# Performance work log

Measured on AMD Instinct MI355X. Metric: run time of the kernel, lower is better.

## Reference

```python
import jax, jax.numpy as jnp
import numpy as np

N, F, C, H, D = 32768, 128, 4, 8, 32
DM = H * D  # 256, d_model
E, B = 65536, 8192


def _pe():
    # sinusoidal positional encoding over the chain dimension, shape [C, DM]
    pos = jnp.arange(C, dtype=jnp.float32)[:, None]
    di = jnp.arange(0, DM, 2, dtype=jnp.float32)[None, :]
    div = 10000.0 ** (di / DM)
    pe = jnp.zeros((C, DM), jnp.float32)
    pe = pe.at[:, 0::2].set(jnp.sin(pos / div))
    pe = pe.at[:, 1::2].set(jnp.cos(pos / div))
    return pe


def _leaky(v):
    return jnp.where(v >= 0, v, 0.2 * v)


def setup_inputs() -> dict:
    key = jax.random.key(0)
    ks = jax.random.split(key, 6)
    x = jax.random.normal(ks[0], (N, F), jnp.float32)
    edge_index = jax.random.randint(ks[1], (2, E), 0, N)
    bridge_index = jax.random.randint(ks[2], (2, B), 0, N)
    W_in = jax.random.normal(ks[3], (DM, F), jnp.float32) * 0.05       # linear_input.weight
    double_attn = jax.random.normal(ks[4], (1, C * H, D), jnp.float32) * 0.1
    W_res = jax.random.normal(ks[5], (C * DM, F), jnp.float32) * 0.05  # residual_linear.weight
    bias = jnp.zeros((C * DM,), jnp.float32)
    prelu_w = jnp.float32(0.25)  # nn.PReLU default
    return {"x": x, "edge_index": edge_index, "bridge_index": bridge_index,
            "W_in": W_in, "double_attn": double_attn, "W_res": W_res,
            "bias": bias, "prelu_w": prelu_w}


def reference(x, edge_index, bridge_index, W_in, double_attn, W_res, bias, prelu_w):
    n = x.shape[0]
    # project + chain positional encoding -> [n, C, H, D]
    xl = x @ W_in.T                                   # [n, DM]
    xr = (xl[:, None, :] + _pe()[None]).reshape(n, C, H, D)

    src_bond, dst_bond = edge_index[0], edge_index[1]
    bond_attn = _leaky(xr[src_bond] + xr[dst_bond])   # [E, C, H, D]

    src_bridge, dst_bridge = bridge_index[0], bridge_index[1]
    ch = jnp.arange(C)
    prev_ch = jnp.clip(ch - 1, 0, None)
    next_ch = jnp.clip(ch + 1, None, C - 1)
    src2dst = _leaky(xr[dst_bridge] + xr[src_bridge][:, next_ch]).at[:, -1].set(0.0)
    dst2src = _leaky(xr[src_bridge] + xr[dst_bridge][:, prev_ch]).at[:, 0].set(0.0)

    full_src = jnp.concatenate([src_bond, src_bridge, dst_bridge])   # [Et]
    full_dst = jnp.concatenate([dst_bond, dst_bridge, src_bridge])   # [Et]
    x_src = jnp.concatenate([xr[src_bond], xr[src_bridge], xr[dst_bridge]], axis=0).reshape(-1, C * H, D)
    edge_attn = jnp.concatenate([bond_attn, src2dst, dst2src], axis=0).reshape(-1, C * H, D)

    scores = (double_attn * edge_attn).sum(-1)        # [Et, C*H]
    exp_s = jnp.exp(scores - scores.max())            # global-max stabilized, as in original
    denom = jax.ops.segment_sum(exp_s, full_dst, num_segments=n)     # [n, C*H]
    alpha = exp_s / (denom[full_dst] + 1e-16)

    # NOTE: faithful to original bug - x_src (per-edge, len Et) indexed by NODE ids
    proj = x_src[full_src] * alpha[..., None]         # [Et, C*H, D]
    out = jax.ops.segment_sum(proj, full_dst, num_segments=n)        # [n, C*H, D]

    out = out + (x @ W_res.T).reshape(n, C * H, D)    # residual
    out = out.reshape(n, C * H * D) + bias            # concat + bias
    out = jnp.where(out >= 0, out, prelu_w * out)     # PReLU
    return out
```

## Files before the change

### kernel.cpp

```cpp
#include <hip/hip_runtime.h>
#include <math.h>

#define N_NODES 32768
#define F_IN    128
#define C_CH    4
#define H_HEADS 8
#define D_DIM   32
#define DM      256
#define E_BOND  65536
#define B_BRIDGE 8192
#define ET      (E_BOND + 2*B_BRIDGE)
#define OUTC    1024
#define CAP     24
#define NCOLS   1280

#define WS_XL      0u
#define WS_PE      33554432u
#define WS_BUCKET4 33558528u
#define WS_CNT     46141440u
#define WS_RESID   46272512u
#define WS_XB      113381376u
#define WS_WC      121769984u

typedef __attribute__((ext_vector_type(8))) short bf16x8;
typedef __attribute__((ext_vector_type(4))) float f32x4;
typedef __attribute__((ext_vector_type(4))) _Float16 f16x4;

__device__ __forceinline__ float leaky(float v) { return v >= 0.f ? v : 0.2f*v; }
__device__ __forceinline__ ushort f2bf(float f) {
    unsigned u = __float_as_uint(f);
    unsigned r = (u + 0x7fffu + ((u >> 16) & 1u)) >> 16;
    return (ushort)r;
}

__device__ __forceinline__ void edge_decode(int e, const int* __restrict__ ei,
                                            const int* __restrict__ bi,
                                            int& nA, int& nB, int& tp) {
    if (e < E_BOND)               { nA = ei[e]; nB = ei[E_BOND + e]; tp = 0; }
    else if (e < E_BOND+B_BRIDGE) { int i = e - E_BOND;
                                    nA = bi[B_BRIDGE + i]; nB = bi[i]; tp = 1; }
    else                          { int i = e - E_BOND - B_BRIDGE;
                                    nA = bi[i]; nB = bi[B_BRIDGE + i]; tp = 2; }
}

__global__ __launch_bounds__(256) void prep_kernel(
        const float* __restrict__ x, const float* __restrict__ W_in,
        const float* __restrict__ W_res, const int* __restrict__ ei,
        const int* __restrict__ bi, ushort* __restrict__ xb,
        ushort* __restrict__ wc, int* __restrict__ counts,
        int4* __restrict__ bucket4, float* __restrict__ pe) {
    const int bid = blockIdx.x;
    const int tid = threadIdx.x;
    if (bid < 4096) {
        const long i = (long)bid*256 + tid;
        float4 v = ((const float4*)x)[i];
        ushort4 o; o.x = f2bf(v.x); o.y = f2bf(v.y); o.z = f2bf(v.z); o.w = f2bf(v.w);
        ((ushort4*)xb)[i] = o;
    } else if (bid < 4256) {
        const int i = (bid - 4096)*256 + tid;
        float4 v = (i < 8192) ? ((const float4*)W_in)[i]
                              : ((const float4*)W_res)[i - 8192];
        ushort4 o; o.x = f2bf(v.x); o.y = f2bf(v.y); o.z = f2bf(v.z); o.w = f2bf(v.w);
        ((ushort4*)wc)[i] = o;
    } else if (bid < 4576) {
        const int e = (bid - 4256)*256 + tid;
        if (e < ET) {
            int nA, nB, tp;
            edge_decode(e, ei, bi, nA, nB, tp);
            const int dst = (tp == 0) ? nB : nA;
            const int fs  = (tp == 0) ? nA : nB;
            const int g   = ei[fs];
            int slot = atomicAdd(&counts[dst], 1);
            if (slot < CAP) bucket4[(long)dst*CAP + slot] = make_int4(nA, nB, g, tp);
        }
    } else {
#pragma unroll
        for (int k = 0; k < 4; ++k) {
            int idx = k*256 + tid;
            int c = idx >> 8, p = idx & 255;
            float expo = (float)(p & ~1) * (1.0f/256.0f);
            float div  = powf(10000.0f, expo);
            float arg  = (float)c / div;
            pe[idx] = (p & 1) ? cosf(arg) : sinf(arg);
        }
    }
}

#define LDSK 72
__global__ __launch_bounds__(256) void mfma_gemm(
        const ushort* __restrict__ xb, const ushort* __restrict__ wc,
        float* __restrict__ xl, _Float16* __restrict__ resid) {
    __shared__ ushort As[128*LDSK];
    __shared__ ushort Bs[128*LDSK];
    const int tid = threadIdx.x;
    const int m0 = blockIdx.x * 128;
    const int n0 = blockIdx.y * 128;
    const int lane = tid & 63, wv = tid >> 6;
    const int wm = wv & 1, wn = wv >> 1;
    const int quad = lane >> 4, l15 = lane & 15;
    const int mbase = wm*64, nbase = wn*64;
    f32x4 acc[4][4] = {};

    for (int kt = 0; kt < 2; ++kt) {
        if (kt) __syncthreads();
#pragma unroll
        for (int i = 0; i < 4; ++i) {
            int c = tid + i*256;
            int row = c >> 3, seg = c & 7;
            *(uint4*)&As[row*LDSK + seg*8] =
                *(const uint4*)(xb + (long)(m0 + row)*F_IN + kt*64 + seg*8);
        }
#pragma unroll
        for (int i = 0; i < 4; ++i) {
            int c = tid + i*256;
            int row = c >> 3, seg = c & 7;
            *(uint4*)&Bs[row*LDSK + seg*8] =
                *(const uint4*)(wc + (long)(n0 + row)*F_IN + kt*64 + seg*8);
        }
        __syncthreads();
#pragma unroll
        for (int ks = 0; ks < 2; ++ks) {
            const int ko = ks*32 + quad*8;
            bf16x8 af[4], bfr[4];
#pragma unroll
            for (int mi = 0; mi < 4; ++mi)
                af[mi] = *(const bf16x8*)&As[(mbase + mi*16 + l15)*LDSK + ko];
#pragma unroll
            for (int ni = 0; ni < 4; ++ni)
                bfr[ni] = *(const bf16x8*)&Bs[(nbase + ni*16 + l15)*LDSK + ko];
#pragma unroll
            for (int mi = 0; mi < 4; ++mi)
#pragma unroll
                for (int ni = 0; ni < 4; ++ni)
                    acc[mi][ni] = __builtin_amdgcn_mfma_f32_16x16x32_bf16(
                        af[mi], bfr[ni], acc[mi][ni], 0, 0, 0);
        }
    }

    if (n0 < DM) {
#pragma unroll
        for (int mi = 0; mi < 4; ++mi) {
            const int mrow = m0 + mbase + mi*16 + quad*4;
#pragma unroll
            for (int ni = 0; ni < 4; ++ni) {
                const int col = n0 + nbase + ni*16 + l15;
#pragma unroll
                for (int r = 0; r < 4; ++r)
                    xl[(long)(mrow + r)*DM + col] = acc[mi][ni][r];
            }
        }
    } else {
        const int coloff = n0 - DM;
#pragma unroll
        for (int mi = 0; mi < 4; ++mi) {
            const int mrow = m0 + mbase + mi*16 + quad*4;
#pragma unroll
            for (int ni = 0; ni < 4; ++ni) {
                const int col = coloff + nbase + ni*16 + l15;
#pragma unroll
                for (int r = 0; r < 4; ++r)
                    resid[(long)(mrow + r)*OUTC + col] = (_Float16)acc[mi][ni][r];
            }
        }
    }
}

__global__ __launch_bounds__(256) void node_kernel(
        const float* __restrict__ xl, const float* __restrict__ pe,
        const float* __restrict__ datt, const int* __restrict__ counts,
        const int4* __restrict__ bucket4, const _Float16* __restrict__ resid,
        const float* __restrict__ bias, const float* __restrict__ pw,
        float* __restrict__ out) {
    const int t = threadIdx.x;
    const int l = t & 63, wv = t >> 6;
    const int n = blockIdx.x*4 + wv;
    const int pos = l * 4;
    const int h = l >> 3, dq = l & 7;
    const int cnt = min(counts[n], CAP);
    const long nb = (long)n*CAP;

    float4 pv[4], w4[4];
#pragma unroll
    for (int c = 0; c < 4; ++c) {
        pv[c] = *(const float4*)(pe + c*DM + pos);
        w4[c] = *(const float4*)(datt + (c*H_HEADS + h)*D_DIM + dq*4);
    }
    f16x4 hv[4]; float4 bv[4];
#pragma unroll
    for (int c = 0; c < 4; ++c) {
        hv[c] = *(const f16x4*)(resid + (long)n*OUTC + c*256 + pos);
        bv[c] = *(const float4*)(bias + c*256 + pos);
    }
    const float w = *pw;

    float m[4]   = {-1e30f, -1e30f, -1e30f, -1e30f};
    float den[4] = {0.f, 0.f, 0.f, 0.f};
    f32x4 acc[4] = {};

    int4 ed;
    if (cnt > 0) ed = bucket4[nb];
    for (int i = 0; i < cnt; ++i) {
        const float4 ua = *(const float4*)(xl + (long)ed.x*DM + pos);
        const float4 ub = *(const float4*)(xl + (long)ed.y*DM + pos);
        const float4 xv = *(const float4*)(xl + (long)ed.z*DM + pos);
        const int tp = ed.w;
        const int nx = (i+1 < cnt) ? i+1 : i;
        ed = bucket4[nb + nx];

        const float sx = ua.x + ub.x;
        const float sy = ua.y + ub.y;
        const float sz = ua.z + ub.z;
        const float sw = ua.w + ub.w;

        float p[4];
#pragma unroll
        for (int c = 0; c < 4; ++c) {
            int cB = (tp == 0) ? c : (tp == 1 ? (c+1 < 3 ? c+1 : 3)
                                              : (c-1 > 0 ? c-1 : 0));
            bool z = (tp == 1 && c == 3) || (tp == 2 && c == 0);
            float4 pa = pv[c];
            float4 pb = (cB == 0) ? pv[0] : (cB == 1) ? pv[1]
                       : (cB == 2) ? pv[2] : pv[3];
            float v0 = leaky(sx + pa.x + pb.x);
            float v1 = leaky(sy + pa.y + pb.y);
            float v2 = leaky(sz + pa.z + pb.z);
            float v3 = leaky(sw + pa.w + pb.w);
            float d = w4[c].x*v0 + w4[c].y*v1 + w4[c].z*v2 + w4[c].w*v3;
            p[c] = z ? 0.f : d;
            p[c] += __shfl_xor(p[c], 1);
            p[c] += __shfl_xor(p[c], 2);
            p[c] += __shfl_xor(p[c], 4);
        }
#pragma unroll
        for (int c = 0; c < 4; ++c) {
            float mn   = fmaxf(m[c], p[c]);
            float corr = __expf(m[c] - mn);
            float ww   = __expf(p[c] - mn);
            den[c] = den[c]*corr + ww;
            acc[c].x = acc[c].x*corr + ww*xv.x;
            acc[c].y = acc[c].y*corr + ww*xv.y;
            acc[c].z = acc[c].z*corr + ww*xv.z;
            acc[c].w = acc[c].w*corr + ww*xv.w;
            m[c] = mn;
        }
    }

#pragma unroll
    for (int c = 0; c < 4; ++c) {
        const float inv = 1.f / (den[c] + 1e-16f);
        float r0 = (acc[c].x + den[c]*pv[c].x)*inv + (float)hv[c].x + bv[c].x;
        float r1 = (acc[c].y + den[c]*pv[c].y)*inv + (float)hv[c].y + bv[c].y;
        float r2 = (acc[c].z + den[c]*pv[c].z)*inv + (float)hv[c].z + bv[c].z;
        float r3 = (acc[c].w + den[c]*pv[c].w)*inv + (float)hv[c].w + bv[c].w;
        r0 = r0 >= 0.f ? r0 : w*r0;
        r1 = r1 >= 0.f ? r1 : w*r1;
        r2 = r2 >= 0.f ? r2 : w*r2;
        r3 = r3 >= 0.f ? r3 : w*r3;
        *(float4*)(out + (long)n*OUTC + c*256 + pos) = make_float4(r0, r1, r2, r3);
    }
}

extern "C" void kernel_launch(void* const* d_in, const int* in_sizes, int n_in,
                              void* d_out, int out_size, void* d_ws, size_t ws_size,
                              hipStream_t stream) {
    const float* x     = (const float*)d_in[0];
    const int*   ei    = (const int*)d_in[1];
    const int*   bi    = (const int*)d_in[2];
    const float* W_in  = (const float*)d_in[3];
    const float* datt  = (const float*)d_in[4];
    const float* W_res = (const float*)d_in[5];
    const float* bias  = (const float*)d_in[6];
    const float* pw    = (const float*)d_in[7];
    float* out = (float*)d_out;
    char*  ws  = (char*)d_ws;

    float*     xl      = (float*)(ws + WS_XL);
    float*     pe      = (float*)(ws + WS_PE);
    int4*      bucket4 = (int4*)(ws + WS_BUCKET4);
    int*       counts  = (int*)(ws + WS_CNT);
    _Float16*  resid   = (_Float16*)(ws + WS_RESID);
    ushort*    xb      = (ushort*)(ws + WS_XB);
    ushort*    wc      = (ushort*)(ws + WS_WC);

    hipMemsetAsync(counts, 0, (size_t)N_NODES*4, stream);
    prep_kernel<<<4577, 256, 0, stream>>>(x, W_in, W_res, ei, bi, xb, wc,
                                          counts, bucket4, pe);
    {
        dim3 grid(N_NODES/128, NCOLS/128);
        mfma_gemm<<<grid, 256, 0, stream>>>(xb, wc, xl, resid);
    }
    node_kernel<<<N_NODES/4, 256, 0, stream>>>(xl, pe, datt, counts, bucket4,
                                               resid, bias, pw, out);
}
```

Measured before the change: 332.6 us.

## Gather bf16 score features, unroll edges by two, persistent node waves

The GEMM now also writes a bf16 copy of the projected features. The node kernel gathers the two score operands from that copy, which halves their bytes, while still reading the aggregated value in fp32. The edge loop is unrolled by two to put more independent gathers in flight, and the node kernel becomes a grid-stride loop over 2048 blocks so per-wave constants load once. This adds an extra 16MB write in the GEMM and bf16 rounding in the attention scores.

```diff
diff --git a/kernel.cpp b/kernel.cpp
--- a/kernel.cpp
+++ b/kernel.cpp
@@ -15,12 +15,13 @@
 #define NCOLS   1280
 
 #define WS_XL      0u
-#define WS_PE      33554432u
-#define WS_BUCKET4 33558528u
-#define WS_CNT     46141440u
-#define WS_RESID   46272512u
-#define WS_XB      113381376u
-#define WS_WC      121769984u
+#define WS_XLB     33554432u
+#define WS_PE      50331648u
+#define WS_BUCKET4 50335744u
+#define WS_CNT     62918656u
+#define WS_RESID   63049728u
+#define WS_XB      130158592u
+#define WS_WC      138547200u
 
 typedef __attribute__((ext_vector_type(8))) short bf16x8;
 typedef __attribute__((ext_vector_type(4))) float f32x4;
@@ -31,6 +32,9 @@
     unsigned u = __float_as_uint(f);
     unsigned r = (u + 0x7fffu + ((u >> 16) & 1u)) >> 16;
     return (ushort)r;
+}
+__device__ __forceinline__ float bf2f(ushort u) {
+    return __uint_as_float((unsigned)u << 16);
 }
 
 __device__ __forceinline__ void edge_decode(int e, const int* __restrict__ ei,
@@ -89,7 +93,8 @@
 #define LDSK 72
 __global__ __launch_bounds__(256) void mfma_gemm(
         const ushort* __restrict__ xb, const ushort* __restrict__ wc,
-        float* __restrict__ xl, _Float16* __restrict__ resid) {
+        float* __restrict__ xl, ushort* __restrict__ xlb,
+        _Float16* __restrict__ resid) {
     __shared__ ushort As[128*LDSK];
     __shared__ ushort Bs[128*LDSK];
     const int tid = threadIdx.x;
@@ -145,8 +150,11 @@
             for (int ni = 0; ni < 4; ++ni) {
                 const int col = n0 + nbase + ni*16 + l15;
 #pragma unroll
-                for (int r = 0; r < 4; ++r)
-                    xl[(long)(mrow + r)*DM + col] = acc[mi][ni][r];
+                for (int r = 0; r < 4; ++r) {
+                    float v = acc[mi][ni][r];
+                    xl [(long)(mrow + r)*DM + col] = v;
+                    xlb[(long)(mrow + r)*DM + col] = f2bf(v);
+                }
             }
         }
     } else {
@@ -166,97 +174,149 @@
 }
 
 __global__ __launch_bounds__(256) void node_kernel(
-        const float* __restrict__ xl, const float* __restrict__ pe,
-        const float* __restrict__ datt, const int* __restrict__ counts,
-        const int4* __restrict__ bucket4, const _Float16* __restrict__ resid,
-        const float* __restrict__ bias, const float* __restrict__ pw,
-        float* __restrict__ out) {
+        const float* __restrict__ xl, const ushort* __restrict__ xlb,
+        const float* __restrict__ pe, const float* __restrict__ datt,
+        const int* __restrict__ counts, const int4* __restrict__ bucket4,
+        const _Float16* __restrict__ resid, const float* __restrict__ bias,
+        const float* __restrict__ pw, float* __restrict__ out) {
     const int t = threadIdx.x;
     const int l = t & 63, wv = t >> 6;
-    const int n = blockIdx.x*4 + wv;
+    const int nwaves = gridDim.x * 4;
+    const int wgid = blockIdx.x*4 + wv;
     const int pos = l * 4;
     const int h = l >> 3, dq = l & 7;
-    const int cnt = min(counts[n], CAP);
-    const long nb = (long)n*CAP;
-
-    float4 pv[4], w4[4];
+
+    float4 pv[4], w4[4], bv[4];
 #pragma unroll
     for (int c = 0; c < 4; ++c) {
         pv[c] = *(const float4*)(pe + c*DM + pos);
         w4[c] = *(const float4*)(datt + (c*H_HEADS + h)*D_DIM + dq*4);
-    }
-    f16x4 hv[4]; float4 bv[4];
-#pragma unroll
-    for (int c = 0; c < 4; ++c) {
-        hv[c] = *(const f16x4*)(resid + (long)n*OUTC + c*256 + pos);
         bv[c] = *(const float4*)(bias + c*256 + pos);
     }
     const float w = *pw;
 
-    float m[4]   = {-1e30f, -1e30f, -1e30f, -1e30f};
-    float den[4] = {0.f, 0.f, 0.f, 0.f};
-    f32x4 acc[4] = {};
-
-    int4 ed;
-    if (cnt > 0) ed = bucket4[nb];
-    for (int i = 0; i < cnt; ++i) {
-        const float4 ua = *(const float4*)(xl + (long)ed.x*DM + pos);
-        const float4 ub = *(const float4*)(xl + (long)ed.y*DM + pos);
-        const float4 xv = *(const float4*)(xl + (long)ed.z*DM + pos);
-        const int tp = ed.w;
-        const int nx = (i+1 < cnt) ? i+1 : i;
-        ed = bucket4[nb + nx];
-
-        const float sx = ua.x + ub.x;
-        const float sy = ua.y + ub.y;
-        const float sz = ua.z + ub.z;
-        const float sw = ua.w + ub.w;
-
-        float p[4];
+    for (int n = wgid; n < N_NODES; n += nwaves) {
+        const int cnt = min(counts[n], CAP);
+        const long nb = (long)n*CAP;
+
+        f16x4 hv[4];
+#pragma unroll
+        for (int c = 0; c < 4; ++c)
+            hv[c] = *(const f16x4*)(resid + (long)n*OUTC + c*256 + pos);
+
+        float m[4]   = {-1e30f, -1e30f, -1e30f, -1e30f};
+        float den[4] = {0.f, 0.f, 0.f, 0.f};
+        f32x4 acc[4] = {};
+
+        int4 edA, edB;
+        if (cnt > 0) edA = bucket4[nb];
+        if (cnt > 1) edB = bucket4[nb + 1];
+
+        for (int i = 0; i < cnt; i += 2) {
+            const ushort4 uaA = *(const ushort4*)(xlb + (long)edA.x*DM + pos);
+            const ushort4 ubA = *(const ushort4*)(xlb + (long)edA.y*DM + pos);
+            const float4  xvA = *(const float4*)(xl + (long)edA.z*DM + pos);
+            const int tpA = edA.w;
+            const bool hasB = (i + 1) < cnt;
+            ushort4 uaB, ubB; float4 xvB; int tpB = 0;
+            if (hasB) {
+                uaB = *(const ushort4*)(xlb + (long)edB.x*DM + pos);
+                ubB = *(const ushort4*)(xlb + (long)edB.y*DM + pos);
+                xvB = *(const float4*)(xl + (long)edB.z*DM + pos);
+                tpB = edB.w;
+            }
+            if (i + 2 < cnt) edA = bucket4[nb + i + 2];
+            if (i + 3 < cnt) edB = bucket4[nb + i + 3];
+
+            {
+                const float sx = bf2f(uaA.x) + bf2f(ubA.x);
+                const float sy = bf2f(uaA.y) + bf2f(ubA.y);
+                const float sz = bf2f(uaA.z) + bf2f(ubA.z);
+                const float sw = bf2f(uaA.w) + bf2f(ubA.w);
+                float p[4];
+#pragma unroll
+                for (int c = 0; c < 4; ++c) {
+                    int cB = (tpA == 0) ? c : (tpA == 1 ? (c+1 < 3 ? c+1 : 3)
+                                                        : (c-1 > 0 ? c-1 : 0));
+                    bool z = (tpA == 1 && c == 3) || (tpA == 2 && c == 0);
+                    float4 pa = pv[c];
+                    float4 pb = (cB == 0) ? pv[0] : (cB == 1) ? pv[1]
+                               : (cB == 2) ? pv[2] : pv[3];
+                    float v0 = leaky(sx + pa.x + pb.x);
+                    float v1 = leaky(sy + pa.y + pb.y);
+                    float v2 = leaky(sz + pa.z + pb.z);
+                    float v3 = leaky(sw + pa.w + pb.w);
+                    float d = w4[c].x*v0 + w4[c].y*v1 + w4[c].z*v2 + w4[c].w*v3;
+                    p[c] = z ? 0.f : d;
+                    p[c] += __shfl_xor(p[c], 1);
+                    p[c] += __shfl_xor(p[c], 2);
+                    p[c] += __shfl_xor(p[c], 4);
+                }
+#pragma unroll
+                for (int c = 0; c < 4; ++c) {
+                    float mn   = fmaxf(m[c], p[c]);
+                    float corr = __expf(m[c] - mn);
+                    float ww   = __expf(p[c] - mn);
+                    den[c] = den[c]*corr + ww;
+                    acc[c].x = acc[c].x*corr + ww*xvA.x;
+                    acc[c].y = acc[c].y*corr + ww*xvA.y;
+                    acc[c].z = acc[c].z*corr + ww*xvA.z;
+                    acc[c].w = acc[c].w*corr + ww*xvA.w;
+                    m[c] = mn;
+                }
+            }
+            if (hasB) {
+                const float sx = bf2f(uaB.x) + bf2f(ubB.x);
+                const float sy = bf2f(uaB.y) + bf2f(ubB.y);
+                const float sz = bf2f(uaB.z) + bf2f(ubB.z);
+                const float sw = bf2f(uaB.w) + bf2f(ubB.w);
+                float p[4];
+#pragma unroll
+                for (int c = 0; c < 4; ++c) {
+                    int cB = (tpB == 0) ? c : (tpB == 1 ? (c+1 < 3 ? c+1 : 3)
+                                                        : (c-1 > 0 ? c-1 : 0));
+                    bool z = (tpB == 1 && c == 3) || (tpB == 2 && c == 0);
+                    float4 pa = pv[c];
+                    float4 pb = (cB == 0) ? pv[0] : (cB == 1) ? pv[1]
+                               : (cB == 2) ? pv[2] : pv[3];
+                    float v0 = leaky(sx + pa.x + pb.x);
+                    float v1 = leaky(sy + pa.y + pb.y);
+                    float v2 = leaky(sz + pa.z + pb.z);
+                    float v3 = leaky(sw + pa.w + pb.w);
+                    float d = w4[c].x*v0 + w4[c].y*v1 + w4[c].z*v2 + w4[c].w*v3;
+                    p[c] = z ? 0.f : d;
+                    p[c] += __shfl_xor(p[c], 1);
+                    p[c] += __shfl_xor(p[c], 2);
+                    p[c] += __shfl_xor(p[c], 4);
+                }
+#pragma unroll
+                for (int c = 0; c < 4; ++c) {
+                    float mn   = fmaxf(m[c], p[c]);
+                    float corr = __expf(m[c] - mn);
+                    float ww   = __expf(p[c] - mn);
+                    den[c] = den[c]*corr + ww;
+                    acc[c].x = acc[c].x*corr + ww*xvB.x;
+                    acc[c].y = acc[c].y*corr + ww*xvB.y;
+                    acc[c].z = acc[c].z*corr + ww*xvB.z;
+                    acc[c].w = acc[c].w*corr + ww*xvB.w;
+                    m[c] = mn;
+                }
+            }
+        }
+
 #pragma unroll
         for (int c = 0; c < 4; ++c) {
-            int cB = (tp == 0) ? c : (tp == 1 ? (c+1 < 3 ? c+1 : 3)
-                                              : (c-1 > 0 ? c-1 : 0));
-            bool z = (tp == 1 && c == 3) || (tp == 2 && c == 0);
-            float4 pa = pv[c];
-            float4 pb = (cB == 0) ? pv[0] : (cB == 1) ? pv[1]
-                       : (cB == 2) ? pv[2] : pv[3];
-            float v0 = leaky(sx + pa.x + pb.x);
-            float v1 = leaky(sy + pa.y + pb.y);
-            float v2 = leaky(sz + pa.z + pb.z);
-            float v3 = leaky(sw + pa.w + pb.w);
-            float d = w4[c].x*v0 + w4[c].y*v1 + w4[c].z*v2 + w4[c].w*v3;
-            p[c] = z ? 0.f : d;
-            p[c] += __shfl_xor(p[c], 1);
-            p[c] += __shfl_xor(p[c], 2);
-            p[c] += __shfl_xor(p[c], 4);
-        }
-#pragma unroll
-        for (int c = 0; c < 4; ++c) {
-            float mn   = fmaxf(m[c], p[c]);
-            float corr = __expf(m[c] - mn);
-            float ww   = __expf(p[c] - mn);
-            den[c] = den[c]*corr + ww;
-            acc[c].x = acc[c].x*corr + ww*xv.x;
-            acc[c].y = acc[c].y*corr + ww*xv.y;
-            acc[c].z = acc[c].z*corr + ww*xv.z;
-            acc[c].w = acc[c].w*corr + ww*xv.w;
-            m[c] = mn;
-        }
-    }
-
-#pragma unroll
-    for (int c = 0; c < 4; ++c) {
-        const float inv = 1.f / (den[c] + 1e-16f);
-        float r0 = (acc[c].x + den[c]*pv[c].x)*inv + (float)hv[c].x + bv[c].x;
-        float r1 = (acc[c].y + den[c]*pv[c].y)*inv + (float)hv[c].y + bv[c].y;
-        float r2 = (acc[c].z + den[c]*pv[c].z)*inv + (float)hv[c].z + bv[c].z;
-        float r3 = (acc[c].w + den[c]*pv[c].w)*inv + (float)hv[c].w + bv[c].w;
-        r0 = r0 >= 0.f ? r0 : w*r0;
-        r1 = r1 >= 0.f ? r1 : w*r1;
-        r2 = r2 >= 0.f ? r2 : w*r2;
-        r3 = r3 >= 0.f ? r3 : w*r3;
-        *(float4*)(out + (long)n*OUTC + c*256 + pos) = make_float4(r0, r1, r2, r3);
+            const float inv = 1.f / (den[c] + 1e-16f);
+            float r0 = (acc[c].x + den[c]*pv[c].x)*inv + (float)hv[c].x + bv[c].x;
+            float r1 = (acc[c].y + den[c]*pv[c].y)*inv + (float)hv[c].y + bv[c].y;
+            float r2 = (acc[c].z + den[c]*pv[c].z)*inv + (float)hv[c].z + bv[c].z;
+            float r3 = (acc[c].w + den[c]*pv[c].w)*inv + (float)hv[c].w + bv[c].w;
+            r0 = r0 >= 0.f ? r0 : w*r0;
+            r1 = r1 >= 0.f ? r1 : w*r1;
+            r2 = r2 >= 0.f ? r2 : w*r2;
+            r3 = r3 >= 0.f ? r3 : w*r3;
+            *(float4*)(out + (long)n*OUTC + c*256 + pos) = make_float4(r0, r1, r2, r3);
+        }
     }
 }
 
@@ -275,6 +335,7 @@
     char*  ws  = (char*)d_ws;
 
     float*     xl      = (float*)(ws + WS_XL);
+    ushort*    xlb     = (ushort*)(ws + WS_XLB);
     float*     pe      = (float*)(ws + WS_PE);
     int4*      bucket4 = (int4*)(ws + WS_BUCKET4);
     int*       counts  = (int*)(ws + WS_CNT);
@@ -287,8 +348,8 @@
                                           counts, bucket4, pe);
     {
         dim3 grid(N_NODES/128, NCOLS/128);
-        mfma_gemm<<<grid, 256, 0, stream>>>(xb, wc, xl, resid);
-    }
-    node_kernel<<<N_NODES/4, 256, 0, stream>>>(xl, pe, datt, counts, bucket4,
-                                               resid, bias, pw, out);
-}
+        mfma_gemm<<<grid, 256, 0, stream>>>(xb, wc, xl, xlb, resid);
+    }
+    node_kernel<<<2048, 256, 0, stream>>>(xl, xlb, pe, datt, counts, bucket4,
+                                          resid, bias, pw, out);
+}
```

Result: faster. 311.0 us (-6.5%).
